# Kernel optimization log

Hardware: AMD Instinct MI355X
Metric: run time of the kernel (lower is better)

## Reference

```python
import jax, jax.numpy as jnp
import numpy as np

H = 16            # num_heads
DK = 64           # head_k_dim = hidden*0.5/H
DV = 128          # head_v_dim = hidden*1.0/H
EPS = 1e-5
GATE_NORM = 16.0


def setup_inputs() -> dict:
    key = jax.random.key(0)
    ks = jax.random.split(key, 8)
    B, T, D = 4, 4096, 2048
    hidden_states = jax.random.normal(ks[0], (B, T, D), jnp.float32)
    state = jax.random.normal(ks[1], (B, H, DK, DV), jnp.float32)
    norm_w = jnp.ones((D,), jnp.float32)
    # fan-in scaled init so activations stay O(1)
    k_w = jax.random.normal(ks[2], (H * DK, D), jnp.float32) / np.sqrt(D)
    v_w = jax.random.normal(ks[3], (H * DV, D), jnp.float32) / np.sqrt(D)
    gk_w1 = jax.random.normal(ks[4], (16, D), jnp.float32) / np.sqrt(D)
    gk_w2 = jax.random.normal(ks[5], (H * DK, 16), jnp.float32) / np.sqrt(16)
    gk_b = jnp.zeros((H * DK,), jnp.float32)
    return {"hidden_states": hidden_states, "state": state, "norm_w": norm_w,
            "k_w": k_w, "v_w": v_w, "gk_w1": gk_w1, "gk_w2": gk_w2, "gk_b": gk_b}


def reference(hidden_states, state, norm_w, k_w, v_w, gk_w1, gk_w2, gk_b):
    B, T, D = hidden_states.shape
    # RMSNorm
    x = hidden_states * jax.lax.rsqrt(jnp.mean(hidden_states * hidden_states, -1, keepdims=True) + EPS)
    x = x * norm_w
    # projections -> [B,T,H,d]
    k = (x @ k_w.T).reshape(B, T, H, DK)
    v = (x @ v_w.T).reshape(B, T, H, DV)
    gk = jax.nn.log_sigmoid((x @ gk_w1.T) @ gk_w2.T + gk_b) / GATE_NORM  # <= 0
    gk = gk.reshape(B, T, H, DK)
    # GLA recurrence S_t = diag(exp(gk_t)) S_{t-1} + k_t^T v_t, unrolled:
    # S_T = exp(G_T) * S_0 + sum_t exp(G_T - G_t) * k_t v_t^T, G_t = cumsum(gk)
    G = jnp.cumsum(gk, axis=1)                       # [B,T,H,DK]
    g_total = G[:, -1]                               # [B,H,DK]
    decay = jnp.exp(G[:, -1:, :, :] - G)             # in (0,1], stable
    new_state = jnp.exp(g_total)[..., None] * state + \
        jnp.einsum('bthk,bthv->bhkv', k * decay, v)
    return new_state
```

## Files before the change

### kernel.cpp

```cpp
#include <hip/hip_runtime.h>

#define B_ 4
#define T_ 4096
#define D_ 2048
#define H_ 16
#define DK_ 64
#define DV_ 128
#define HDK 1024
#define HDV 2048
#define NN 3072
#define MM 16384
#define NT_ 32

typedef unsigned short u16;
typedef unsigned int u32;
typedef __attribute__((ext_vector_type(8))) short bf16x8;
typedef __attribute__((ext_vector_type(4))) float f32x4;

typedef const __attribute__((address_space(1))) u16 gu16;
typedef __attribute__((address_space(3))) u16 lu16;

__device__ __forceinline__ float b2f(u16 u) {
  u32 x = ((u32)u) << 16; float f; __builtin_memcpy(&f, &x, 4); return f;
}
__device__ __forceinline__ u16 f2b(float f) {
  u32 x; __builtin_memcpy(&x, &f, 4);
  u32 r = x + 0x7FFFu + ((x >> 16) & 1u);
  return (u16)(r >> 16);
}
__device__ __forceinline__ float fexp(float x) { return exp2f(x * 1.44269504f); }
__device__ __forceinline__ float flogsig(float z) {
  float u = exp2f(-fabsf(z) * 1.44269504f);
  float l = log2f(1.f + u) * 0.69314718f;
  return fminf(z, 0.f) - l;
}

__global__ __launch_bounds__(256) void k_cvtw(const float* __restrict__ kw,
                                              const float* __restrict__ vw,
                                              u16* __restrict__ Wb) {
  int i = blockIdx.x * 256 + threadIdx.x;
  size_t e = (size_t)i * 8;
  const float* src = (e < (size_t)HDK * D_) ? (kw + e) : (vw + (e - (size_t)HDK * D_));
  float4 f0 = ((const float4*)src)[0];
  float4 f1 = ((const float4*)src)[1];
  union { int4 v; u16 u[8]; } o;
  o.u[0] = f2b(f0.x); o.u[1] = f2b(f0.y); o.u[2] = f2b(f0.z); o.u[3] = f2b(f0.w);
  o.u[4] = f2b(f1.x); o.u[5] = f2b(f1.y); o.u[6] = f2b(f1.z); o.u[7] = f2b(f1.w);
  *(int4*)(Wb + e) = o.v;
}

__global__ __launch_bounds__(256) void k_rms(const float* __restrict__ hs,
                                             const float* __restrict__ nw,
                                             const float* __restrict__ w1,
                                             u16* __restrict__ xb,
                                             float* __restrict__ y) {
  int r0 = blockIdx.x * 4;
  int tid = threadIdx.x;
  int wv = tid >> 6, ln = tid & 63;
  __shared__ float red[4][4];
  __shared__ float ys[4][4][16];
  float x[4][8];
  float ssq[4];
  #pragma unroll
  for (int r = 0; r < 4; ++r) {
    const float4* hp = (const float4*)(hs + (size_t)(r0 + r) * D_);
    float4 a = hp[tid * 2], b = hp[tid * 2 + 1];
    x[r][0] = a.x; x[r][1] = a.y; x[r][2] = a.z; x[r][3] = a.w;
    x[r][4] = b.x; x[r][5] = b.y; x[r][6] = b.z; x[r][7] = b.w;
    float s = 0.f;
    #pragma unroll
    for (int i = 0; i < 8; ++i) s += x[r][i] * x[r][i];
    #pragma unroll
    for (int o = 32; o > 0; o >>= 1) s += __shfl_xor(s, o, 64);
    ssq[r] = s;
  }
  if (ln == 0) {
    #pragma unroll
    for (int r = 0; r < 4; ++r) red[wv][r] = ssq[r];
  }
  __syncthreads();
  const float4* np_ = (const float4*)nw;
  float4 n0 = np_[tid * 2], n1 = np_[tid * 2 + 1];
  float nwv[8] = {n0.x, n0.y, n0.z, n0.w, n1.x, n1.y, n1.z, n1.w};
  #pragma unroll
  for (int r = 0; r < 4; ++r) {
    float tot = red[0][r] + red[1][r] + red[2][r] + red[3][r];
    float inv = rsqrtf(tot * (1.f / D_) + 1e-5f);
    union { int4 v; u16 u[8]; } o;
    #pragma unroll
    for (int i = 0; i < 8; ++i) { x[r][i] = x[r][i] * inv * nwv[i]; o.u[i] = f2b(x[r][i]); }
    *(int4*)(xb + (size_t)(r0 + r) * D_ + tid * 8) = o.v;
  }
  float p[4][16];
  #pragma unroll
  for (int r = 0; r < 4; ++r)
    #pragma unroll
    for (int j = 0; j < 16; ++j) p[r][j] = 0.f;
  #pragma unroll
  for (int j = 0; j < 16; ++j) {
    const float4* wp = (const float4*)(w1 + (size_t)j * D_);
    float4 a = wp[tid * 2], b = wp[tid * 2 + 1];
    float wj[8] = {a.x, a.y, a.z, a.w, b.x, b.y, b.z, b.w};
    #pragma unroll
    for (int r = 0; r < 4; ++r) {
      float s = 0.f;
      #pragma unroll
      for (int i = 0; i < 8; ++i) s += x[r][i] * wj[i];
      p[r][j] = s;
    }
  }
  #pragma unroll
  for (int r = 0; r < 4; ++r)
    #pragma unroll
    for (int j = 0; j < 16; ++j) {
      float s = p[r][j];
      #pragma unroll
      for (int o = 32; o > 0; o >>= 1) s += __shfl_xor(s, o, 64);
      p[r][j] = s;
    }
  if (ln == 0) {
    for (int r = 0; r < 4; ++r)
      for (int j = 0; j < 16; ++j) ys[wv][r][j] = p[r][j];
  }
  __syncthreads();
  if (tid < 64) {
    int r = tid >> 4, j = tid & 15;
    y[(size_t)(r0 + r) * 16 + j] = ys[0][r][j] + ys[1][r][j] + ys[2][r][j] + ys[3][r][j];
  }
}

#define GLDS(SRC, DST) __builtin_amdgcn_global_load_lds((gu16*)(SRC), (lu16*)(DST), 16, 0, 0)

#define HALFSTEP(DB, KH, NB, KTN, VMSTR, DO_STAGE) do {                        \
    if (DO_STAGE) {                                                            \
      const u16* a_ = Ag + (size_t)(KTN) * 64 + (KH) * 32;                     \
      const u16* b_ = Bg + (size_t)(KTN) * 64 + (KH) * 32;                     \
      GLDS(a_,            &SA[NB][KH][lw]);                                    \
      GLDS(a_ + 16 * D_,  &SA[NB][KH][lw + 512]);                              \
      GLDS(b_,            &SB[NB][KH][lw]);                                    \
      GLDS(b_ + 16 * D_,  &SB[NB][KH][lw + 512]);                              \
    }                                                                          \
    asm volatile("s_waitcnt vmcnt(" VMSTR ")" ::: "memory");                   \
    __builtin_amdgcn_s_barrier();                                              \
    __builtin_amdgcn_sched_barrier(0);                                         \
    bf16x8 bfr[4];                                                             \
    _Pragma("unroll")                                                          \
    for (int ni = 0; ni < 4; ++ni)                                             \
      bfr[ni] = *(const bf16x8*)&SB[DB][KH][(wc * 64 + ni * 16 + r) * 32 + kcol]; \
    bf16x8 afr[8];                                                             \
    _Pragma("unroll")                                                          \
    for (int mi = 0; mi < 8; ++mi)                                             \
      afr[mi] = *(const bf16x8*)&SA[DB][KH][(wr * 128 + mi * 16 + r) * 32 + kcol]; \
    __builtin_amdgcn_s_setprio(1);                                             \
    _Pragma("unroll")                                                          \
    for (int mi = 0; mi < 8; ++mi)                                             \
      _Pragma("unroll")                                                        \
      for (int ni = 0; ni < 4; ++ni)                                           \
        acc[mi][ni] = __builtin_amdgcn_mfma_f32_16x16x32_bf16(afr[mi], bfr[ni], acc[mi][ni], 0, 0, 0); \
    __builtin_amdgcn_s_setprio(0);                                             \
  } while (0)

__global__ __launch_bounds__(512, 2) void k_gemm(const u16* __restrict__ X,
                                                 const u16* __restrict__ W,
                                                 u16* __restrict__ C) {
  __shared__ u16 SA[2][2][8192];
  __shared__ u16 SB[2][2][8192];
  int bid = blockIdx.x;
  int swzb = (bid & 7) * 96 + (bid >> 3);
  int tm = swzb / 12, tn = swzb - tm * 12;
  int m0 = tm << 8, n0 = tn << 8;
  int tid = threadIdx.x;
  int w = tid >> 6, l = tid & 63;
  int wr = w >> 2, wc = w & 3;
  int arow = w * 32 + (l >> 2);
  int csw = 8 * ((l & 3) ^ ((l >> 3) & 3));
  const u16* Ag = X + (size_t)(m0 + arow) * D_ + csw;
  const u16* Bg = W + (size_t)(n0 + arow) * D_ + csw;
  int lw = w * 1024;
  int r = l & 15, kq = l >> 4;
  int kcol = 8 * (kq ^ ((r >> 1) & 3));

  f32x4 acc[8][4];
  #pragma unroll
  for (int mi = 0; mi < 8; ++mi)
    #pragma unroll
    for (int ni = 0; ni < 4; ++ni)
      #pragma unroll
      for (int q = 0; q < 4; ++q) acc[mi][ni][q] = 0.f;

  #pragma unroll
  for (int kh = 0; kh < 2; ++kh) {
    GLDS(Ag + kh * 32,           &SA[0][kh][lw]);
    GLDS(Ag + kh * 32 + 16 * D_, &SA[0][kh][lw + 512]);
    GLDS(Bg + kh * 32,           &SB[0][kh][lw]);
    GLDS(Bg + kh * 32 + 16 * D_, &SB[0][kh][lw + 512]);
  }

  for (int kt = 0; kt < NT_ - 1; ++kt) {
    int db = kt & 1, nb = db ^ 1;
    HALFSTEP(db, 0, nb, kt + 1, "8", 1);
    HALFSTEP(db, 1, nb, kt + 1, "8", 1);
  }
  HALFSTEP(1, 0, 0, 0, "4", 0);
  HALFSTEP(1, 1, 0, 0, "0", 0);

  int cr = (l >> 4) * 4, cc = l & 15;
  #pragma unroll
  for (int mi = 0; mi < 8; ++mi)
    #pragma unroll
    for (int ni = 0; ni < 4; ++ni)
      #pragma unroll
      for (int q = 0; q < 4; ++q) {
        int gm = m0 + wr * 128 + mi * 16 + cr + q;
        int gn = n0 + wc * 64 + ni * 16 + cc;
        C[(size_t)gm * NN + gn] = f2b(acc[mi][ni][q]);
      }
}

__global__ __launch_bounds__(256) void k_gkcs(const float* __restrict__ y,
                                              const float* __restrict__ w2,
                                              const float* __restrict__ gb,
                                              u16* __restrict__ gkh,
                                              float* __restrict__ ct) {
  __shared__ float yl[64][16];
  int blk = blockIdx.x;
  int cg = blk & 3, tc = (blk >> 2) & 63, b = blk >> 8;
  int tid = threadIdx.x;
  int c = cg * 256 + tid;
  {
    int row = tid >> 2, q = tid & 3;
    const float4* src = (const float4*)(y + (size_t)(b * T_ + tc * 64 + row) * 16 + q * 4);
    *(float4*)&yl[row][q * 4] = *src;
  }
  float w2r[16];
  {
    const float4* wsrc = (const float4*)(w2 + (size_t)c * 16);
    float4 q0 = wsrc[0], q1 = wsrc[1], q2 = wsrc[2], q3 = wsrc[3];
    w2r[0] = q0.x; w2r[1] = q0.y; w2r[2] = q0.z; w2r[3] = q0.w;
    w2r[4] = q1.x; w2r[5] = q1.y; w2r[6] = q1.z; w2r[7] = q1.w;
    w2r[8] = q2.x; w2r[9] = q2.y; w2r[10] = q2.z; w2r[11] = q2.w;
    w2r[12] = q3.x; w2r[13] = q3.y; w2r[14] = q3.z; w2r[15] = q3.w;
  }
  float gbr = gb[c];
  __syncthreads();
  float sum = 0.f;
  size_t rowbase = (size_t)(b * T_ + tc * 64) * HDK + c;
  for (int t = 0; t < 64; ++t) {
    const float4* yv4 = (const float4*)&yl[t][0];
    float4 y0 = yv4[0], y1 = yv4[1], y2 = yv4[2], y3 = yv4[3];
    float z = gbr;
    z = fmaf(y0.x, w2r[0], z);  z = fmaf(y0.y, w2r[1], z);
    z = fmaf(y0.z, w2r[2], z);  z = fmaf(y0.w, w2r[3], z);
    z = fmaf(y1.x, w2r[4], z);  z = fmaf(y1.y, w2r[5], z);
    z = fmaf(y1.z, w2r[6], z);  z = fmaf(y1.w, w2r[7], z);
    z = fmaf(y2.x, w2r[8], z);  z = fmaf(y2.y, w2r[9], z);
    z = fmaf(y2.z, w2r[10], z); z = fmaf(y2.w, w2r[11], z);
    z = fmaf(y3.x, w2r[12], z); z = fmaf(y3.y, w2r[13], z);
    z = fmaf(y3.z, w2r[14], z); z = fmaf(y3.w, w2r[15], z);
    float g = flogsig(z) * (1.f / 16.f);
    _Float16 hv = (_Float16)g;
    u16 bits; __builtin_memcpy(&bits, &hv, 2);
    gkh[rowbase + (size_t)t * HDK] = bits;
    sum += (float)hv;
  }
  ct[(size_t)(b * 64 + tc) * HDK + c] = sum;
}

__global__ __launch_bounds__(256) void k_scan(const float* __restrict__ ct,
                                              float* __restrict__ co,
                                              float* __restrict__ gt) {
  int b = blockIdx.x >> 2, cg = blockIdx.x & 3;
  int c = cg * 256 + threadIdx.x;
  float run = 0.f;
  #pragma unroll 8
  for (int tc = 0; tc < 64; ++tc) {
    size_t idx = (size_t)(b * 64 + tc) * HDK + c;
    co[idx] = run;
    run += ct[idx];
  }
  gt[b * HDK + c] = run;
}

__global__ __launch_bounds__(256) void k_decay(const u16* __restrict__ gkh,
                                               const float* __restrict__ co,
                                               const float* __restrict__ gt,
                                               const u16* __restrict__ kv,
                                               u16* __restrict__ Ab) {
  int blk = blockIdx.x;
  int cg = blk & 3, tc = (blk >> 2) & 63, b = blk >> 8;
  int c = cg * 256 + threadIdx.x;
  float run = co[(size_t)(b * 64 + tc) * HDK + c];
  float g = gt[b * HDK + c];
  #pragma unroll 8
  for (int tt = 0; tt < 64; ++tt) {
    size_t row = (size_t)(b * T_) + tc * 64 + tt;
    u16 bits = gkh[row * HDK + c];
    _Float16 hv; __builtin_memcpy(&hv, &bits, 2);
    run += (float)hv;
    float decay = fexp(g - run);
    float kvl = b2f(kv[row * NN + c]);
    Ab[row * HDK + c] = f2b(kvl * decay);
  }
}

__global__ __launch_bounds__(256) void k_outer(const u16* __restrict__ Ab,
                                               const u16* __restrict__ kv,
                                               float* __restrict__ part) {
  __shared__ u16 At[2][64][40];
  __shared__ u16 Vt[2][128][40];
  int s = blockIdx.x, h = blockIdx.y, b = blockIdx.z;
  int tid = threadIdx.x;
  int w = tid >> 6, l = tid & 63;
  int adk = tid & 63, atq = tid >> 6;
  int vdv = tid & 127, vth = tid >> 7;
  int r = l & 15, q = l >> 4;
  f32x4 acc[8];
  #pragma unroll
  for (int n = 0; n < 8; ++n)
    #pragma unroll
    for (int j = 0; j < 4; ++j) acc[n][j] = 0.f;

  union { int4 v[2]; u16 u[16]; } vbuf;
  union { int4 v; u16 u[8]; } abuf;

  #define LOADT(KK) do {                                                              \
      int t0_ = s * 256 + (KK) * 32;                                                  \
      _Pragma("unroll")                                                               \
      for (int i = 0; i < 8; ++i)                                                     \
        abuf.u[i] = Ab[(size_t)(b * T_ + t0_ + atq * 8 + i) * HDK + h * DK_ + adk];   \
      _Pragma("unroll")                                                               \
      for (int i = 0; i < 16; ++i)                                                    \
        vbuf.u[i] = kv[(size_t)(b * T_ + t0_ + vth * 16 + i) * NN + HDK + h * DV_ + vdv]; \
    } while (0)

  #define WRITET(BF) do {                                                             \
      *(int4*)&At[BF][adk][atq * 8] = abuf.v;                                         \
      *(int4*)&Vt[BF][vdv][vth * 16] = vbuf.v[0];                                     \
      *(int4*)&Vt[BF][vdv][vth * 16 + 8] = vbuf.v[1];                                 \
    } while (0)

  LOADT(0);
  WRITET(0);
  for (int kk = 0; kk < 8; ++kk) {
    int cur = kk & 1;
    if (kk < 7) LOADT(kk + 1);
    __syncthreads();
    bf16x8 af = *(const bf16x8*)&At[cur][w * 16 + r][q * 8];
    #pragma unroll
    for (int n = 0; n < 8; ++n) {
      bf16x8 vf = *(const bf16x8*)&Vt[cur][n * 16 + r][q * 8];
      acc[n] = __builtin_amdgcn_mfma_f32_16x16x32_bf16(af, vf, acc[n], 0, 0, 0);
    }
    __syncthreads();
    if (kk < 7) WRITET(1 - cur);
  }
  #undef LOADT
  #undef WRITET

  float* dst = part + ((size_t)(b * H_ + h) * 16 + s) * (DK_ * DV_);
  #pragma unroll
  for (int n = 0; n < 8; ++n)
    #pragma unroll
    for (int j = 0; j < 4; ++j)
      dst[(w * 16 + q * 4 + j) * DV_ + n * 16 + r] = acc[n][j];
}

__global__ __launch_bounds__(256) void k_final(const float* __restrict__ part,
                                               const float* __restrict__ gt,
                                               const float* __restrict__ st,
                                               float* __restrict__ out) {
  int i = blockIdx.x * 256 + threadIdx.x;
  int dv = i & 127, dk = (i >> 7) & 63, h = (i >> 13) & 15, b = i >> 17;
  size_t base = ((size_t)(b * H_ + h) * 16) * 8192 + dk * DV_ + dv;
  float s = 0.f;
  #pragma unroll
  for (int sp = 0; sp < 16; ++sp) s += part[base + (size_t)sp * 8192];
  float g = gt[b * HDK + h * DK_ + dk];
  out[i] = fexp(g) * st[i] + s;
}

extern "C" void kernel_launch(void* const* d_in, const int* in_sizes, int n_in,
                              void* d_out, int out_size, void* d_ws, size_t ws_size,
                              hipStream_t stream) {
  const float* hs = (const float*)d_in[0];
  const float* st = (const float*)d_in[1];
  const float* nw = (const float*)d_in[2];
  const float* kw = (const float*)d_in[3];
  const float* vw = (const float*)d_in[4];
  const float* w1 = (const float*)d_in[5];
  const float* w2 = (const float*)d_in[6];
  const float* gb = (const float*)d_in[7];
  float* out = (float*)d_out;
  char* ws = (char*)d_ws;

  u16*  Wb  = (u16*)(ws + 0);
  u16*  xb  = (u16*)(ws + 12582912);
  float* y  = (float*)(ws + 79691776);
  u16*  kv  = (u16*)(ws + 80740352);
  u16*  gkh = (u16*)(ws + 181403648);
  float* ct = (float*)(ws + 214958080);
  float* co = (float*)(ws + 216006656);
  float* gt = (float*)(ws + 217055232);
  u16*  Ab  = (u16*)(ws + 12582912);
  float* part = (float*)(ws + 12582912 + 33554432);

  k_cvtw<<<dim3(3072), dim3(256), 0, stream>>>(kw, vw, Wb);
  k_rms<<<dim3(4096), dim3(256), 0, stream>>>(hs, nw, w1, xb, y);
  k_gemm<<<dim3(768), dim3(512), 0, stream>>>(xb, Wb, kv);
  k_gkcs<<<dim3(1024), dim3(256), 0, stream>>>(y, w2, gb, gkh, ct);
  k_scan<<<dim3(16), dim3(256), 0, stream>>>(ct, co, gt);
  k_decay<<<dim3(1024), dim3(256), 0, stream>>>(gkh, co, gt, kv, Ab);
  k_outer<<<dim3(16, 16, 4), dim3(256), 0, stream>>>(Ab, kv, part);
  k_final<<<dim3(2048), dim3(256), 0, stream>>>(part, gt, st, out);
}
```

Measured before the change: 369.6 us.

## Interleave LDS fragment loads with staged global loads in GEMM; halve outer splits

Result: no change. 365.0 us (median of 2 runs) (-1.2%).

```diff
diff --git a/kernel.cpp b/kernel.cpp
--- a/kernel.cpp
+++ b/kernel.cpp
@@ -131,33 +131,63 @@
 
 #define GLDS(SRC, DST) __builtin_amdgcn_global_load_lds((gu16*)(SRC), (lu16*)(DST), 16, 0, 0)
 
-#define HALFSTEP(DB, KH, NB, KTN, VMSTR, DO_STAGE) do {                        \
-    if (DO_STAGE) {                                                            \
-      const u16* a_ = Ag + (size_t)(KTN) * 64 + (KH) * 32;                     \
-      const u16* b_ = Bg + (size_t)(KTN) * 64 + (KH) * 32;                     \
-      GLDS(a_,            &SA[NB][KH][lw]);                                    \
-      GLDS(a_ + 16 * D_,  &SA[NB][KH][lw + 512]);                              \
-      GLDS(b_,            &SB[NB][KH][lw]);                                    \
-      GLDS(b_ + 16 * D_,  &SB[NB][KH][lw + 512]);                              \
-    }                                                                          \
-    asm volatile("s_waitcnt vmcnt(" VMSTR ")" ::: "memory");                   \
+#define MFMA16(AF, MB) do {                                                    \
+    __builtin_amdgcn_s_setprio(1);                                             \
+    _Pragma("unroll")                                                          \
+    for (int mi_ = 0; mi_ < 4; ++mi_)                                          \
+      _Pragma("unroll")                                                        \
+      for (int ni_ = 0; ni_ < 4; ++ni_)                                        \
+        acc[(MB) + mi_][ni_] = __builtin_amdgcn_mfma_f32_16x16x32_bf16(        \
+            AF[mi_], bf[ni_], acc[(MB) + mi_][ni_], 0, 0, 0);                  \
+    __builtin_amdgcn_s_setprio(0);                                             \
+    __builtin_amdgcn_sched_barrier(0);                                         \
+  } while (0)
+
+#define KTILE(DB, NB, VM0, VM2, ST) do {                                       \
+           \
+    asm volatile("s_waitcnt vmcnt(" VM0 ")" ::: "memory");                     \
     __builtin_amdgcn_s_barrier();                                              \
     __builtin_amdgcn_sched_barrier(0);                                         \
-    bf16x8 bfr[4];                                                             \
-    _Pragma("unroll")                                                          \
-    for (int ni = 0; ni < 4; ++ni)                                             \
-      bfr[ni] = *(const bf16x8*)&SB[DB][KH][(wc * 64 + ni * 16 + r) * 32 + kcol]; \
-    bf16x8 afr[8];                                                             \
-    _Pragma("unroll")                                                          \
-    for (int mi = 0; mi < 8; ++mi)                                             \
-      afr[mi] = *(const bf16x8*)&SA[DB][KH][(wr * 128 + mi * 16 + r) * 32 + kcol]; \
-    __builtin_amdgcn_s_setprio(1);                                             \
-    _Pragma("unroll")                                                          \
-    for (int mi = 0; mi < 8; ++mi)                                             \
-      _Pragma("unroll")                                                        \
-      for (int ni = 0; ni < 4; ++ni)                                           \
-        acc[mi][ni] = __builtin_amdgcn_mfma_f32_16x16x32_bf16(afr[mi], bfr[ni], acc[mi][ni], 0, 0, 0); \
-    __builtin_amdgcn_s_setprio(0);                                             \
+    _Pragma("unroll")                                                          \
+    for (int mi_ = 0; mi_ < 4; ++mi_)                                          \
+      af[mi_] = *(const bf16x8*)&SA[DB][0][(wr * 128 + mi_ * 16 + r) * 32 + kcol]; \
+    _Pragma("unroll")                                                          \
+    for (int ni_ = 0; ni_ < 4; ++ni_)                                          \
+      bf[ni_] = *(const bf16x8*)&SB[DB][0][(wc * 64 + ni_ * 16 + r) * 32 + kcol]; \
+    if (ST) { GLDS(An, &SA[NB][0][lw]); GLDS(An + 16 * D_, &SA[NB][0][lw + 512]); } \
+    asm volatile("s_waitcnt lgkmcnt(0)" ::: "memory");                         \
+    __builtin_amdgcn_sched_barrier(0);                                         \
+    MFMA16(af, 0);                                                             \
+                  \
+    _Pragma("unroll")                                                          \
+    for (int mi_ = 0; mi_ < 4; ++mi_)                                          \
+      af2[mi_] = *(const bf16x8*)&SA[DB][0][(wr * 128 + (4 + mi_) * 16 + r) * 32 + kcol]; \
+    if (ST) { GLDS(An + 32, &SA[NB][1][lw]); GLDS(An + 32 + 16 * D_, &SA[NB][1][lw + 512]); } \
+    asm volatile("s_waitcnt lgkmcnt(0)" ::: "memory");                         \
+    __builtin_amdgcn_sched_barrier(0);                                         \
+    MFMA16(af2, 4);                                                            \
+                       \
+    asm volatile("s_waitcnt vmcnt(" VM2 ")" ::: "memory");                     \
+    __builtin_amdgcn_s_barrier();                                              \
+    __builtin_amdgcn_sched_barrier(0);                                         \
+    _Pragma("unroll")                                                          \
+    for (int mi_ = 0; mi_ < 4; ++mi_)                                          \
+      af[mi_] = *(const bf16x8*)&SA[DB][1][(wr * 128 + mi_ * 16 + r) * 32 + kcol]; \
+    _Pragma("unroll")                                                          \
+    for (int ni_ = 0; ni_ < 4; ++ni_)                                          \
+      bf[ni_] = *(const bf16x8*)&SB[DB][1][(wc * 64 + ni_ * 16 + r) * 32 + kcol]; \
+    if (ST) { GLDS(Bn, &SB[NB][0][lw]); GLDS(Bn + 16 * D_, &SB[NB][0][lw + 512]); } \
+    asm volatile("s_waitcnt lgkmcnt(0)" ::: "memory");                         \
+    __builtin_amdgcn_sched_barrier(0);                                         \
+    MFMA16(af, 0);                                                             \
+                             \
+    _Pragma("unroll")                                                          \
+    for (int mi_ = 0; mi_ < 4; ++mi_)                                          \
+      af2[mi_] = *(const bf16x8*)&SA[DB][1][(wr * 128 + (4 + mi_) * 16 + r) * 32 + kcol]; \
+    if (ST) { GLDS(Bn + 32, &SB[NB][1][lw]); GLDS(Bn + 32 + 16 * D_, &SB[NB][1][lw + 512]); } \
+    asm volatile("s_waitcnt lgkmcnt(0)" ::: "memory");                         \
+    __builtin_amdgcn_sched_barrier(0);                                         \
+    MFMA16(af2, 4);                                                            \
   } while (0)
 
 __global__ __launch_bounds__(512, 2) void k_gemm(const u16* __restrict__ X,
@@ -188,21 +218,24 @@
       #pragma unroll
       for (int q = 0; q < 4; ++q) acc[mi][ni][q] = 0.f;
 
-  #pragma unroll
-  for (int kh = 0; kh < 2; ++kh) {
-    GLDS(Ag + kh * 32,           &SA[0][kh][lw]);
-    GLDS(Ag + kh * 32 + 16 * D_, &SA[0][kh][lw + 512]);
-    GLDS(Bg + kh * 32,           &SB[0][kh][lw]);
-    GLDS(Bg + kh * 32 + 16 * D_, &SB[0][kh][lw + 512]);
-  }
+  bf16x8 af[4], af2[4], bf[4];
+
+  GLDS(Ag,           &SA[0][0][lw]);  GLDS(Ag + 16 * D_,      &SA[0][0][lw + 512]);
+  GLDS(Ag + 32,      &SA[0][1][lw]);  GLDS(Ag + 32 + 16 * D_, &SA[0][1][lw + 512]);
+  GLDS(Bg,           &SB[0][0][lw]);  GLDS(Bg + 16 * D_,      &SB[0][0][lw + 512]);
+  GLDS(Bg + 32,      &SB[0][1][lw]);  GLDS(Bg + 32 + 16 * D_, &SB[0][1][lw + 512]);
 
   for (int kt = 0; kt < NT_ - 1; ++kt) {
     int db = kt & 1, nb = db ^ 1;
-    HALFSTEP(db, 0, nb, kt + 1, "8", 1);
-    HALFSTEP(db, 1, nb, kt + 1, "8", 1);
-  }
-  HALFSTEP(1, 0, 0, 0, "4", 0);
-  HALFSTEP(1, 1, 0, 0, "0", 0);
+    const u16* An = Ag + (size_t)(kt + 1) * 64;
+    const u16* Bn = Bg + (size_t)(kt + 1) * 64;
+    KTILE(db, nb, "2", "4", 1);
+  }
+  {
+    const u16* An = Ag;
+    const u16* Bn = Bg;
+    KTILE(1, 0, "2", "0", 0);
+  }
 
   int cr = (l >> 4) * 4, cc = l & 15;
   #pragma unroll
@@ -324,7 +357,7 @@
   union { int4 v; u16 u[8]; } abuf;
 
   #define LOADT(KK) do {                                                              \
-      int t0_ = s * 256 + (KK) * 32;                                                  \
+      int t0_ = s * 512 + (KK) * 32;                                                  \
       _Pragma("unroll")                                                               \
       for (int i = 0; i < 8; ++i)                                                     \
         abuf.u[i] = Ab[(size_t)(b * T_ + t0_ + atq * 8 + i) * HDK + h * DK_ + adk];   \
@@ -341,9 +374,9 @@
 
   LOADT(0);
   WRITET(0);
-  for (int kk = 0; kk < 8; ++kk) {
+  for (int kk = 0; kk < 16; ++kk) {
     int cur = kk & 1;
-    if (kk < 7) LOADT(kk + 1);
+    if (kk < 15) LOADT(kk + 1);
     __syncthreads();
     bf16x8 af = *(const bf16x8*)&At[cur][w * 16 + r][q * 8];
     #pragma unroll
@@ -352,12 +385,12 @@
       acc[n] = __builtin_amdgcn_mfma_f32_16x16x32_bf16(af, vf, acc[n], 0, 0, 0);
     }
     __syncthreads();
-    if (kk < 7) WRITET(1 - cur);
+    if (kk < 15) WRITET(1 - cur);
   }
   #undef LOADT
   #undef WRITET
 
-  float* dst = part + ((size_t)(b * H_ + h) * 16 + s) * (DK_ * DV_);
+  float* dst = part + ((size_t)(b * H_ + h) * 8 + s) * (DK_ * DV_);
   #pragma unroll
   for (int n = 0; n < 8; ++n)
     #pragma unroll
@@ -371,10 +404,10 @@
                                                float* __restrict__ out) {
   int i = blockIdx.x * 256 + threadIdx.x;
   int dv = i & 127, dk = (i >> 7) & 63, h = (i >> 13) & 15, b = i >> 17;
-  size_t base = ((size_t)(b * H_ + h) * 16) * 8192 + dk * DV_ + dv;
+  size_t base = ((size_t)(b * H_ + h) * 8) * 8192 + dk * DV_ + dv;
   float s = 0.f;
   #pragma unroll
-  for (int sp = 0; sp < 16; ++sp) s += part[base + (size_t)sp * 8192];
+  for (int sp = 0; sp < 8; ++sp) s += part[base + (size_t)sp * 8192];
   float g = gt[b * HDK + h * DK_ + dk];
   out[i] = fexp(g) * st[i] + s;
 }
@@ -410,6 +443,6 @@
   k_gkcs<<<dim3(1024), dim3(256), 0, stream>>>(y, w2, gb, gkh, ct);
   k_scan<<<dim3(16), dim3(256), 0, stream>>>(ct, co, gt);
   k_decay<<<dim3(1024), dim3(256), 0, stream>>>(gkh, co, gt, kv, Ab);
-  k_outer<<<dim3(16, 16, 4), dim3(256), 0, stream>>>(Ab, kv, part);
+  k_outer<<<dim3(8, 16, 4), dim3(256), 0, stream>>>(Ab, kv, part);
   k_final<<<dim3(2048), dim3(256), 0, stream>>>(part, gt, st, out);
 }
```

## Switch GEMM to 32x32x16 MFMA with early prefetch; halve outer-product splits

Applied to the files above, without the earlier changes.

Result: slower. 377.0 us (+2.0%).

```diff
diff --git a/kernel.cpp b/kernel.cpp
--- a/kernel.cpp
+++ b/kernel.cpp
@@ -16,6 +16,7 @@
 typedef unsigned int u32;
 typedef __attribute__((ext_vector_type(8))) short bf16x8;
 typedef __attribute__((ext_vector_type(4))) float f32x4;
+typedef __attribute__((ext_vector_type(16))) float f32x16;
 
 typedef const __attribute__((address_space(1))) u16 gu16;
 typedef __attribute__((address_space(3))) u16 lu16;
@@ -131,33 +132,46 @@
 
 #define GLDS(SRC, DST) __builtin_amdgcn_global_load_lds((gu16*)(SRC), (lu16*)(DST), 16, 0, 0)
 
-#define HALFSTEP(DB, KH, NB, KTN, VMSTR, DO_STAGE) do {                        \
-    if (DO_STAGE) {                                                            \
-      const u16* a_ = Ag + (size_t)(KTN) * 64 + (KH) * 32;                     \
-      const u16* b_ = Bg + (size_t)(KTN) * 64 + (KH) * 32;                     \
-      GLDS(a_,            &SA[NB][KH][lw]);                                    \
-      GLDS(a_ + 16 * D_,  &SA[NB][KH][lw + 512]);                              \
-      GLDS(b_,            &SB[NB][KH][lw]);                                    \
-      GLDS(b_ + 16 * D_,  &SB[NB][KH][lw + 512]);                              \
-    }                                                                          \
+#define PHASE32(DB, KH, VMSTR, DO_ST, STBASE) do {                             \
     asm volatile("s_waitcnt vmcnt(" VMSTR ")" ::: "memory");                   \
     __builtin_amdgcn_s_barrier();                                              \
     __builtin_amdgcn_sched_barrier(0);                                         \
-    bf16x8 bfr[4];                                                             \
+    bf16x8 a_[4][2], b_[2][2];                                                 \
     _Pragma("unroll")                                                          \
-    for (int ni = 0; ni < 4; ++ni)                                             \
-      bfr[ni] = *(const bf16x8*)&SB[DB][KH][(wc * 64 + ni * 16 + r) * 32 + kcol]; \
-    bf16x8 afr[8];                                                             \
+    for (int mt = 0; mt < 4; ++mt)                                             \
+      _Pragma("unroll")                                                        \
+      for (int ks = 0; ks < 2; ++ks) {                                         \
+        int ra = wr * 128 + mt * 32 + l31;                                     \
+        int col = 8 * (((ks << 1) | lh) ^ ((ra >> 1) & 3));                    \
+        a_[mt][ks] = *(const bf16x8*)&SA[DB][KH][ra * 32 + col];               \
+      }                                                                        \
     _Pragma("unroll")                                                          \
-    for (int mi = 0; mi < 8; ++mi)                                             \
-      afr[mi] = *(const bf16x8*)&SA[DB][KH][(wr * 128 + mi * 16 + r) * 32 + kcol]; \
+    for (int nt = 0; nt < 2; ++nt)                                             \
+      _Pragma("unroll")                                                        \
+      for (int ks = 0; ks < 2; ++ks) {                                         \
+        int rb = wc * 64 + nt * 32 + l31;                                      \
+        int col = 8 * (((ks << 1) | lh) ^ ((rb >> 1) & 3));                    \
+        b_[nt][ks] = *(const bf16x8*)&SB[DB][KH][rb * 32 + col];               \
+      }                                                                        \
+    if (DO_ST) {                                                               \
+      GLDS((STBASE) + (KH) * 32,            &SA[DB ^ 1][KH][lw]);              \
+      GLDS((STBASE) + (KH) * 32 + 16 * D_,  &SA[DB ^ 1][KH][lw + 512]);        \
+      GLDS((STBASE##B) + (KH) * 32,           &SB[DB ^ 1][KH][lw]);            \
+      GLDS((STBASE##B) + (KH) * 32 + 16 * D_, &SB[DB ^ 1][KH][lw + 512]);      \
+    }                                                                          \
+    asm volatile("s_waitcnt lgkmcnt(0)" ::: "memory");                         \
+    __builtin_amdgcn_sched_barrier(0);                                         \
     __builtin_amdgcn_s_setprio(1);                                             \
     _Pragma("unroll")                                                          \
-    for (int mi = 0; mi < 8; ++mi)                                             \
+    for (int ks = 0; ks < 2; ++ks)                                             \
       _Pragma("unroll")                                                        \
-      for (int ni = 0; ni < 4; ++ni)                                           \
-        acc[mi][ni] = __builtin_amdgcn_mfma_f32_16x16x32_bf16(afr[mi], bfr[ni], acc[mi][ni], 0, 0, 0); \
+      for (int mt = 0; mt < 4; ++mt)                                           \
+        _Pragma("unroll")                                                      \
+        for (int nt = 0; nt < 2; ++nt)                                         \
+          acc[mt][nt] = __builtin_amdgcn_mfma_f32_32x32x16_bf16(               \
+              a_[mt][ks], b_[nt][ks], acc[mt][nt], 0, 0, 0);                   \
     __builtin_amdgcn_s_setprio(0);                                             \
+    __builtin_amdgcn_sched_barrier(0);                                         \
   } while (0)
 
 __global__ __launch_bounds__(512, 2) void k_gemm(const u16* __restrict__ X,
@@ -172,48 +186,49 @@
   int tid = threadIdx.x;
   int w = tid >> 6, l = tid & 63;
   int wr = w >> 2, wc = w & 3;
+  int l31 = l & 31, lh = l >> 5;
   int arow = w * 32 + (l >> 2);
   int csw = 8 * ((l & 3) ^ ((l >> 3) & 3));
   const u16* Ag = X + (size_t)(m0 + arow) * D_ + csw;
   const u16* Bg = W + (size_t)(n0 + arow) * D_ + csw;
   int lw = w * 1024;
-  int r = l & 15, kq = l >> 4;
-  int kcol = 8 * (kq ^ ((r >> 1) & 3));
-
-  f32x4 acc[8][4];
-  #pragma unroll
-  for (int mi = 0; mi < 8; ++mi)
-    #pragma unroll
-    for (int ni = 0; ni < 4; ++ni)
+
+  f32x16 acc[4][2];
+  #pragma unroll
+  for (int mt = 0; mt < 4; ++mt)
+    #pragma unroll
+    for (int nt = 0; nt < 2; ++nt)
       #pragma unroll
-      for (int q = 0; q < 4; ++q) acc[mi][ni][q] = 0.f;
-
-  #pragma unroll
-  for (int kh = 0; kh < 2; ++kh) {
-    GLDS(Ag + kh * 32,           &SA[0][kh][lw]);
-    GLDS(Ag + kh * 32 + 16 * D_, &SA[0][kh][lw + 512]);
-    GLDS(Bg + kh * 32,           &SB[0][kh][lw]);
-    GLDS(Bg + kh * 32 + 16 * D_, &SB[0][kh][lw + 512]);
-  }
+      for (int q = 0; q < 16; ++q) acc[mt][nt][q] = 0.f;
+
+  GLDS(Ag,      &SA[0][0][lw]);  GLDS(Ag + 16 * D_,      &SA[0][0][lw + 512]);
+  GLDS(Bg,      &SB[0][0][lw]);  GLDS(Bg + 16 * D_,      &SB[0][0][lw + 512]);
+  GLDS(Ag + 32, &SA[0][1][lw]);  GLDS(Ag + 32 + 16 * D_, &SA[0][1][lw + 512]);
+  GLDS(Bg + 32, &SB[0][1][lw]);  GLDS(Bg + 32 + 16 * D_, &SB[0][1][lw + 512]);
 
   for (int kt = 0; kt < NT_ - 1; ++kt) {
-    int db = kt & 1, nb = db ^ 1;
-    HALFSTEP(db, 0, nb, kt + 1, "8", 1);
-    HALFSTEP(db, 1, nb, kt + 1, "8", 1);
-  }
-  HALFSTEP(1, 0, 0, 0, "4", 0);
-  HALFSTEP(1, 1, 0, 0, "0", 0);
-
-  int cr = (l >> 4) * 4, cc = l & 15;
-  #pragma unroll
-  for (int mi = 0; mi < 8; ++mi)
-    #pragma unroll
-    for (int ni = 0; ni < 4; ++ni)
+    int db = kt & 1;
+    const u16* An = Ag + (size_t)(kt + 1) * 64;
+    const u16* AnB = Bg + (size_t)(kt + 1) * 64;
+    PHASE32(db, 0, "4", 1, An);
+    PHASE32(db, 1, "4", 1, An);
+  }
+  {
+    const u16* An = Ag;
+    const u16* AnB = Bg;
+    PHASE32(1, 0, "4", 0, An);
+    PHASE32(1, 1, "0", 0, An);
+  }
+
+  #pragma unroll
+  for (int mt = 0; mt < 4; ++mt)
+    #pragma unroll
+    for (int nt = 0; nt < 2; ++nt)
       #pragma unroll
-      for (int q = 0; q < 4; ++q) {
-        int gm = m0 + wr * 128 + mi * 16 + cr + q;
-        int gn = n0 + wc * 64 + ni * 16 + cc;
-        C[(size_t)gm * NN + gn] = f2b(acc[mi][ni][q]);
+      for (int q = 0; q < 16; ++q) {
+        int gm = m0 + wr * 128 + mt * 32 + (q & 3) + 8 * (q >> 2) + 4 * lh;
+        int gn = n0 + wc * 64 + nt * 32 + l31;
+        C[(size_t)gm * NN + gn] = f2b(acc[mt][nt][q]);
       }
 }
 
@@ -324,7 +339,7 @@
   union { int4 v; u16 u[8]; } abuf;
 
   #define LOADT(KK) do {                                                              \
-      int t0_ = s * 256 + (KK) * 32;                                                  \
+      int t0_ = s * 512 + (KK) * 32;                                                  \
       _Pragma("unroll")                                                               \
       for (int i = 0; i < 8; ++i)                                                     \
         abuf.u[i] = Ab[(size_t)(b * T_ + t0_ + atq * 8 + i) * HDK + h * DK_ + adk];   \
@@ -341,9 +356,9 @@
 
   LOADT(0);
   WRITET(0);
-  for (int kk = 0; kk < 8; ++kk) {
+  for (int kk = 0; kk < 16; ++kk) {
     int cur = kk & 1;
-    if (kk < 7) LOADT(kk + 1);
+    if (kk < 15) LOADT(kk + 1);
     __syncthreads();
     bf16x8 af = *(const bf16x8*)&At[cur][w * 16 + r][q * 8];
     #pragma unroll
@@ -352,12 +367,12 @@
       acc[n] = __builtin_amdgcn_mfma_f32_16x16x32_bf16(af, vf, acc[n], 0, 0, 0);
     }
     __syncthreads();
-    if (kk < 7) WRITET(1 - cur);
+    if (kk < 15) WRITET(1 - cur);
   }
   #undef LOADT
   #undef WRITET
 
-  float* dst = part + ((size_t)(b * H_ + h) * 16 + s) * (DK_ * DV_);
+  float* dst = part + ((size_t)(b * H_ + h) * 8 + s) * (DK_ * DV_);
   #pragma unroll
   for (int n = 0; n < 8; ++n)
     #pragma unroll
@@ -371,10 +386,10 @@
                                                float* __restrict__ out) {
   int i = blockIdx.x * 256 + threadIdx.x;
   int dv = i & 127, dk = (i >> 7) & 63, h = (i >> 13) & 15, b = i >> 17;
-  size_t base = ((size_t)(b * H_ + h) * 16) * 8192 + dk * DV_ + dv;
+  size_t base = ((size_t)(b * H_ + h) * 8) * 8192 + dk * DV_ + dv;
   float s = 0.f;
   #pragma unroll
-  for (int sp = 0; sp < 16; ++sp) s += part[base + (size_t)sp * 8192];
+  for (int sp = 0; sp < 8; ++sp) s += part[base + (size_t)sp * 8192];
   float g = gt[b * HDK + h * DK_ + dk];
   out[i] = fexp(g) * st[i] + s;
 }
@@ -410,6 +425,6 @@
   k_gkcs<<<dim3(1024), dim3(256), 0, stream>>>(y, w2, gb, gkh, ct);
   k_scan<<<dim3(16), dim3(256), 0, stream>>>(ct, co, gt);
   k_decay<<<dim3(1024), dim3(256), 0, stream>>>(gkh, co, gt, kv, Ab);
-  k_outer<<<dim3(16, 16, 4), dim3(256), 0, stream>>>(Ab, kv, part);
+  k_outer<<<dim3(8, 16, 4), dim3(256), 0, stream>>>(Ab, kv, part);
   k_final<<<dim3(2048), dim3(256), 0, stream>>>(part, gt, st, out);
 }
```
